# Kernel tuning notes

Hardware: AMD Instinct MI355X
Metric: run time of the kernel (lower is better)

Reference implementation:

```python
import jax, jax.numpy as jnp
import numpy as np

N_NODES = 40000


def _sage_conv(x, edge_index, W_l, W_r, b, num_nodes):
    # PyG SAGEConv (mean aggr): out = lin_l(mean_{j in N(i)} x_j) + lin_r(x_i)
    src, dst = edge_index[0], edge_index[1]
    msgs = x[src]                                            # [E, F] gather
    sums = jax.ops.segment_sum(msgs, dst, num_segments=num_nodes)
    counts = jax.ops.segment_sum(jnp.ones((src.shape[0],), x.dtype), dst,
                                 num_segments=num_nodes)
    mean = sums / jnp.maximum(counts, 1.0)[:, None]          # [N, F]
    return mean @ W_l + b + x @ W_r


def setup_inputs() -> dict:
    key = jax.random.key(0)
    ks = jax.random.split(key, 8)
    in_c, hid_c, out_c = 128, 256, 128
    x = jax.random.normal(ks[0], (N_NODES, in_c), dtype=jnp.float32)
    edge_index = jax.random.randint(ks[1], (2, 640000), 0, N_NODES, dtype=jnp.int64)
    s1 = 1.0 / np.sqrt(in_c)
    s2 = 1.0 / np.sqrt(hid_c)
    return {
        "x": x,
        "edge_index": edge_index,
        "W1_l": jax.random.uniform(ks[2], (in_c, hid_c), jnp.float32, -s1, s1),
        "W1_r": jax.random.uniform(ks[3], (in_c, hid_c), jnp.float32, -s1, s1),
        "b1": jnp.zeros((hid_c,), jnp.float32),
        "W2_l": jax.random.uniform(ks[4], (hid_c, out_c), jnp.float32, -s2, s2),
        "W2_r": jax.random.uniform(ks[5], (hid_c, out_c), jnp.float32, -s2, s2),
        "b2": jnp.zeros((out_c,), jnp.float32),
    }


def reference(x, edge_index, W1_l, W1_r, b1, W2_l, W2_r, b2):
    h = _sage_conv(x, edge_index, W1_l, W1_r, b1, N_NODES)
    h = jax.nn.relu(h)
    out = _sage_conv(h, edge_index, W2_l, W2_r, b2, N_NODES)
    return out
```

## Files before the change

### kernel.cpp

```cpp
#include <hip/hip_runtime.h>


constexpr int F1  = 128;
constexpr int HID = 256;

typedef __attribute__((ext_vector_type(8))) short   short8;
typedef __attribute__((ext_vector_type(8))) ushort  us8;
typedef __attribute__((ext_vector_type(4))) ushort  us4;
typedef __attribute__((ext_vector_type(4))) float   f32x4;

__device__ __forceinline__ ushort f2bf(float f) {
  unsigned u = __float_as_uint(f);
  return (ushort)((u + 0x7fffu + ((u >> 16) & 1u)) >> 16);
}
__device__ __forceinline__ float bf2f_lo(unsigned v) { return __uint_as_float(v << 16); }
__device__ __forceinline__ float bf2f_hi(unsigned v) { return __uint_as_float(v & 0xffff0000u); }

#define GLOAD_LDS16(gsrc, ldst)                                                  \
  __builtin_amdgcn_global_load_lds(                                              \
      (const __attribute__((address_space(1))) void*)(gsrc),                     \
      (__attribute__((address_space(3))) void*)(ldst), 16, 0, 0)

__global__ void prep_kernel(const float* __restrict__ x, ushort* __restrict__ Ab,
                            int* __restrict__ deg,
                            const float* __restrict__ W1l, const float* __restrict__ W1r,
                            const float* __restrict__ W2l, const float* __restrict__ W2r,
                            ushort* __restrict__ B1t, ushort* __restrict__ B2t, int N) {
  int i = blockIdx.x * blockDim.x + threadIdx.x;
  if (i < N) deg[i] = 0;
  if (i < N * 16) {
    int row = i >> 4, c = (i & 15) * 8;
    const float* p = x + (size_t)row * F1 + c;
    us8 o;
#pragma unroll
    for (int j = 0; j < 8; ++j) o[j] = f2bf(p[j]);
    *(us8*)(Ab + (size_t)row * HID + 128 + c) = o;
    return;
  }
  int j = i - N * 16;
  if (j >= 16384) return;
  int which = j >> 13;
  int jj = j & 8191;
  int n = jj >> 5;
  int kb = (jj & 31) * 8;
  us8 o;
  if (which == 0) {
#pragma unroll
    for (int q = 0; q < 8; ++q) {
      int k = kb + q;
      float v = (k < 128) ? W1l[k * HID + n] : W1r[(k - 128) * HID + n];
      o[q] = f2bf(v);
    }
    *(us8*)(B1t + n * HID + kb) = o;
  } else {
#pragma unroll
    for (int q = 0; q < 8; ++q) {
      int k = kb + q;
      float v = (n < 128) ? W2l[k * F1 + n] : W2r[k * F1 + (n - 128)];
      o[q] = f2bf(v);
    }
    *(us8*)(B2t + n * HID + kb) = o;
  }
}

__global__ void deg_kernel(const int* __restrict__ dst, int* __restrict__ deg, int E) {
  int i = (blockIdx.x * blockDim.x + threadIdx.x) * 4;
  if (i + 3 < E) {
    int4 d = *(const int4*)(dst + i);
    atomicAdd(deg + d.x, 1);
    atomicAdd(deg + d.y, 1);
    atomicAdd(deg + d.z, 1);
    atomicAdd(deg + d.w, 1);
  } else {
    for (int q = i; q < E && q < i + 4; ++q) atomicAdd(deg + dst[q], 1);
  }
}

__global__ __launch_bounds__(256) void scan_part(const int* __restrict__ deg,
                                                 int* __restrict__ bsum, int N) {
  __shared__ int sm[256];
  int t = threadIdx.x;
  int base = blockIdx.x * 1024 + t * 4;
  int s = 0;
  if (base + 3 < N) {
    int4 v = *(const int4*)(deg + base);
    s = v.x + v.y + v.z + v.w;
  } else {
    for (int q = 0; q < 4; ++q) if (base + q < N) s += deg[base + q];
  }
  sm[t] = s;
  __syncthreads();
  for (int d = 128; d; d >>= 1) {
    if (t < d) sm[t] += sm[t + d];
    __syncthreads();
  }
  if (t == 0) bsum[blockIdx.x] = sm[0];
}

__global__ __launch_bounds__(256) void scan_emit(const int* __restrict__ deg,
                                                 const int* __restrict__ bsum,
                                                 int* __restrict__ off,
                                                 int* __restrict__ cursor, int N, int nb) {
  __shared__ int sm[256];
  __shared__ int sboff;
  int t = threadIdx.x;
  if (t < 64) {
    int v = (t < nb) ? bsum[t] : 0;
    int inc = v;
    for (int d = 1; d < 64; d <<= 1) {
      int u = __shfl_up(inc, d);
      if (t >= d) inc += u;
    }
    if (t == (int)blockIdx.x) sboff = inc - v;
    if ((int)blockIdx.x == (int)gridDim.x - 1 && t == 63) off[N] = inc;
  }
  int base = blockIdx.x * 1024 + t * 4;
  int d0 = 0, d1 = 0, d2 = 0, d3 = 0;
  if (base + 3 < N) {
    int4 v = *(const int4*)(deg + base);
    d0 = v.x; d1 = v.y; d2 = v.z; d3 = v.w;
  } else {
    if (base + 0 < N) d0 = deg[base + 0];
    if (base + 1 < N) d1 = deg[base + 1];
    if (base + 2 < N) d2 = deg[base + 2];
    if (base + 3 < N) d3 = deg[base + 3];
  }
  int s = d0 + d1 + d2 + d3;
  sm[t] = s;
  __syncthreads();
  for (int d = 1; d < 256; d <<= 1) {
    int u = (t >= d) ? sm[t - d] : 0;
    __syncthreads();
    sm[t] += u;
    __syncthreads();
  }
  int o0 = (t ? sm[t - 1] : 0) + sboff;
  int o1 = o0 + d0, o2 = o1 + d1, o3 = o2 + d2;
  if (base + 3 < N) {
    int4 o = make_int4(o0, o1, o2, o3);
    *(int4*)(off + base) = o;
    *(int4*)(cursor + base) = o;
  } else {
    if (base + 0 < N) { off[base + 0] = o0; cursor[base + 0] = o0; }
    if (base + 1 < N) { off[base + 1] = o1; cursor[base + 1] = o1; }
    if (base + 2 < N) { off[base + 2] = o2; cursor[base + 2] = o2; }
    if (base + 3 < N) { off[base + 3] = o3; cursor[base + 3] = o3; }
  }
}

__global__ void fill_kernel(const int* __restrict__ src, const int* __restrict__ dst,
                            int* __restrict__ cursor, int* __restrict__ csr, int E) {
  int i = (blockIdx.x * blockDim.x + threadIdx.x) * 2;
  if (i + 1 < E) {
    int2 d = *(const int2*)(dst + i);
    int2 s = *(const int2*)(src + i);
    int p0 = atomicAdd(cursor + d.x, 1);
    csr[p0] = s.x;
    int p1 = atomicAdd(cursor + d.y, 1);
    csr[p1] = s.y;
  } else if (i < E) {
    int p = atomicAdd(cursor + dst[i], 1);
    csr[p] = src[i];
  }
}

__device__ __forceinline__ void acc8(float* acc, const uint4 v) {
  acc[0] += bf2f_lo(v.x); acc[1] += bf2f_hi(v.x);
  acc[2] += bf2f_lo(v.y); acc[3] += bf2f_hi(v.y);
  acc[4] += bf2f_lo(v.z); acc[5] += bf2f_hi(v.z);
  acc[6] += bf2f_lo(v.w); acc[7] += bf2f_hi(v.w);
}

__global__ __launch_bounds__(256) void agg1_kernel(const int* __restrict__ off,
                                                   const int* __restrict__ csr,
                                                   ushort* __restrict__ Ab, int N) {
  const int t = threadIdx.x;
  const int w = t >> 6, l = t & 63;
  const int g = l >> 4, sub = l & 15;
  const int node = blockIdx.x * 16 + w * 4 + g;
  if (node >= N) return;
  const int s = off[node], e = off[node + 1];
  float acc[8] = {0.f, 0.f, 0.f, 0.f, 0.f, 0.f, 0.f, 0.f};
  const int cb = sub * 8;
  const int4* csr4 = (const int4*)csr;
  int k0 = s & ~7;
  int4 c0 = csr4[(k0 >> 2) + 0];
  int4 c1 = csr4[(k0 >> 2) + 1];
#define ROW1(j) (*(const uint4*)(Ab + (size_t)(j) * HID + 128 + cb))
  for (int k = k0; k < e; k += 8) {
    int4 n0 = csr4[(k >> 2) + 2];
    int4 n1 = csr4[(k >> 2) + 3];
    if (k + 0 >= s && k + 0 < e) acc8(acc, ROW1(c0.x));
    if (k + 1 >= s && k + 1 < e) acc8(acc, ROW1(c0.y));
    if (k + 2 >= s && k + 2 < e) acc8(acc, ROW1(c0.z));
    if (k + 3 >= s && k + 3 < e) acc8(acc, ROW1(c0.w));
    if (k + 4 >= s && k + 4 < e) acc8(acc, ROW1(c1.x));
    if (k + 5 >= s && k + 5 < e) acc8(acc, ROW1(c1.y));
    if (k + 6 >= s && k + 6 < e) acc8(acc, ROW1(c1.z));
    if (k + 7 < e)               acc8(acc, ROW1(c1.w));
    c0 = n0; c1 = n1;
  }
#undef ROW1
  int d = e - s; if (d < 1) d = 1;
  float inv = 1.0f / (float)d;
  us8 o;
#pragma unroll
  for (int q = 0; q < 8; ++q) o[q] = f2bf(acc[q] * inv);
  *(us8*)(Ab + (size_t)node * HID + cb) = o;
}

__global__ __launch_bounds__(256) void agg2_kernel(const ushort* __restrict__ y2,
                                                   const int* __restrict__ off,
                                                   const int* __restrict__ csr,
                                                   float* __restrict__ out, int N) {
  const int t = threadIdx.x;
  const int w = t >> 6, l = t & 63;
  const int g = l >> 4, sub = l & 15;
  const int node = blockIdx.x * 16 + w * 4 + g;
  if (node >= N) return;
  const int s = off[node], e = off[node + 1];
  float acc[8] = {0.f, 0.f, 0.f, 0.f, 0.f, 0.f, 0.f, 0.f};
  const int cb = sub * 8;
  const int4* csr4 = (const int4*)csr;
  int k0 = s & ~7;
  int4 c0 = csr4[(k0 >> 2) + 0];
  int4 c1 = csr4[(k0 >> 2) + 1];
#define ROW2(j) (*(const uint4*)(y2 + (size_t)(j) * F1 + cb))
  for (int k = k0; k < e; k += 8) {
    int4 n0 = csr4[(k >> 2) + 2];
    int4 n1 = csr4[(k >> 2) + 3];
    if (k + 0 >= s && k + 0 < e) acc8(acc, ROW2(c0.x));
    if (k + 1 >= s && k + 1 < e) acc8(acc, ROW2(c0.y));
    if (k + 2 >= s && k + 2 < e) acc8(acc, ROW2(c0.z));
    if (k + 3 >= s && k + 3 < e) acc8(acc, ROW2(c0.w));
    if (k + 4 >= s && k + 4 < e) acc8(acc, ROW2(c1.x));
    if (k + 5 >= s && k + 5 < e) acc8(acc, ROW2(c1.y));
    if (k + 6 >= s && k + 6 < e) acc8(acc, ROW2(c1.z));
    if (k + 7 < e)               acc8(acc, ROW2(c1.w));
    c0 = n0; c1 = n1;
  }
#undef ROW2
  int d = e - s; if (d < 1) d = 1;
  float inv = 1.0f / (float)d;
  float* po = out + (size_t)node * F1 + cb;
  float4 z0 = *(const float4*)(po);
  float4 z1 = *(const float4*)(po + 4);
  z0.x += acc[0] * inv; z0.y += acc[1] * inv; z0.z += acc[2] * inv; z0.w += acc[3] * inv;
  z1.x += acc[4] * inv; z1.y += acc[5] * inv; z1.z += acc[6] * inv; z1.w += acc[7] * inv;
  *(float4*)(po)     = z0;
  *(float4*)(po + 4) = z1;
}

__global__ __launch_bounds__(256) void mlp_kernel(
    const ushort* __restrict__ A, const ushort* __restrict__ B1t,
    const ushort* __restrict__ B2t, const float* __restrict__ b1,
    const float* __restrict__ b2, ushort* __restrict__ y2,
    float* __restrict__ outp, int M) {
  constexpr int K = 256, BK = 64;
  __shared__ __align__(16) ushort hs[64 * 256];
  __shared__ __align__(16) ushort xreg[4096 + 16384];
  ushort* As  = xreg;
  ushort* B1s = xreg + 4096;
  ushort* B2s = xreg;
  const int t = threadIdx.x;
  const int l = t & 63;
  const int w = t >> 6;
  const int m0 = blockIdx.x * 64;
  const int wc = w * 64;
  const int sk = (((l & 7) ^ (l >> 3)) << 3);
  const int rsub = l >> 3;

  f32x4 acc[4][4];
  const f32x4 zero = {0.f, 0.f, 0.f, 0.f};
#pragma unroll
  for (int mi = 0; mi < 4; ++mi)
#pragma unroll
    for (int ni = 0; ni < 4; ++ni) acc[mi][ni] = zero;

  for (int k0 = 0; k0 < K; k0 += BK) {
    if (k0) __syncthreads();
#pragma unroll
    for (int q = 0; q < 2; ++q) {
      int r = w * 16 + q * 8 + rsub;
      int ar = m0 + r; if (ar >= M) ar = M - 1;
      GLOAD_LDS16(A + (size_t)ar * K + k0 + sk, &As[w * 1024 + q * 512]);
    }
#pragma unroll
    for (int q = 0; q < 8; ++q) {
      int r = w * 64 + q * 8 + rsub;
      GLOAD_LDS16(B1t + (size_t)r * K + k0 + sk, &B1s[w * 4096 + q * 512]);
    }
    __syncthreads();
#pragma unroll
    for (int ks = 0; ks < 2; ++ks) {
      short8 af[4], bfr[4];
      const int kin = ks * 64 + ((l >> 4) << 4);
#pragma unroll
      for (int i = 0; i < 4; ++i) {
        int rA = i * 16 + (l & 15);
        af[i] = *(const short8*)((const char*)As + rA * 128 + (kin ^ ((rA & 7) << 4)));
        int rB = wc + i * 16 + (l & 15);
        bfr[i] = *(const short8*)((const char*)B1s + rB * 128 + (kin ^ ((rB & 7) << 4)));
      }
#pragma unroll
      for (int mi = 0; mi < 4; ++mi)
#pragma unroll
        for (int ni = 0; ni < 4; ++ni)
          acc[mi][ni] = __builtin_amdgcn_mfma_f32_16x16x32_bf16(bfr[ni], af[mi], acc[mi][ni], 0, 0, 0);
    }
  }
#pragma unroll
  for (int ni = 0; ni < 4; ++ni) {
    const int cn = wc + ni * 16 + ((l >> 4) << 2);
    float4 bb = *(const float4*)(b1 + cn);
#pragma unroll
    for (int mi = 0; mi < 4; ++mi) {
      int row = mi * 16 + (l & 15);
      f32x4 v = acc[mi][ni];
      unsigned p0 = (unsigned)f2bf(fmaxf(v[0] + bb.x, 0.f)) |
                    ((unsigned)f2bf(fmaxf(v[1] + bb.y, 0.f)) << 16);
      unsigned p1 = (unsigned)f2bf(fmaxf(v[2] + bb.z, 0.f)) |
                    ((unsigned)f2bf(fmaxf(v[3] + bb.w, 0.f)) << 16);
      int byte = row * 512 + ((2 * cn) ^ ((row & 7) << 4));
      uint2 pk; pk.x = p0; pk.y = p1;
      *(uint2*)((char*)hs + byte) = pk;
      acc[mi][ni] = zero;
    }
  }
  __syncthreads();

  for (int k0 = 0; k0 < K; k0 += BK) {
    if (k0) __syncthreads();
#pragma unroll
    for (int q = 0; q < 8; ++q) {
      int r = w * 64 + q * 8 + rsub;
      GLOAD_LDS16(B2t + (size_t)r * K + k0 + sk, &B2s[w * 4096 + q * 512]);
    }
    __syncthreads();
#pragma unroll
    for (int ks = 0; ks < 2; ++ks) {
      short8 af[4], bfr[4];
      const int kin = ks * 64 + ((l >> 4) << 4);
#pragma unroll
      for (int i = 0; i < 4; ++i) {
        int rA = i * 16 + (l & 15);
        af[i] = *(const short8*)((const char*)hs + rA * 512 + ((2 * k0 + kin) ^ ((rA & 7) << 4)));
        int rB = wc + i * 16 + (l & 15);
        bfr[i] = *(const short8*)((const char*)B2s + rB * 128 + (kin ^ ((rB & 7) << 4)));
      }
#pragma unroll
      for (int mi = 0; mi < 4; ++mi)
#pragma unroll
        for (int ni = 0; ni < 4; ++ni)
          acc[mi][ni] = __builtin_amdgcn_mfma_f32_16x16x32_bf16(bfr[ni], af[mi], acc[mi][ni], 0, 0, 0);
    }
  }
#pragma unroll
  for (int ni = 0; ni < 4; ++ni) {
    const int cn = wc + ni * 16 + ((l >> 4) << 2);
    if (wc < 128) {
#pragma unroll
      for (int mi = 0; mi < 4; ++mi) {
        int row = m0 + mi * 16 + (l & 15);
        if (row >= M) continue;
        f32x4 v = acc[mi][ni];
        us4 o;
        o[0] = f2bf(v[0]); o[1] = f2bf(v[1]); o[2] = f2bf(v[2]); o[3] = f2bf(v[3]);
        *(us4*)(y2 + (size_t)row * F1 + cn) = o;
      }
    } else {
      float4 bb = *(const float4*)(b2 + (cn - 128));
#pragma unroll
      for (int mi = 0; mi < 4; ++mi) {
        int row = m0 + mi * 16 + (l & 15);
        if (row >= M) continue;
        f32x4 v = acc[mi][ni];
        float4 o;
        o.x = v[0] + bb.x; o.y = v[1] + bb.y; o.z = v[2] + bb.z; o.w = v[3] + bb.w;
        *(float4*)(outp + (size_t)row * F1 + (cn - 128)) = o;
      }
    }
  }
}

extern "C" void kernel_launch(void* const* d_in, const int* in_sizes, int n_in,
                              void* d_out, int out_size, void* d_ws, size_t ws_size,
                              hipStream_t stream) {
  const float* x   = (const float*)d_in[0];
  const int* edge  = (const int*)d_in[1];
  const float* W1l = (const float*)d_in[2];
  const float* W1r = (const float*)d_in[3];
  const float* b1  = (const float*)d_in[4];
  const float* W2l = (const float*)d_in[5];
  const float* W2r = (const float*)d_in[6];
  const float* b2  = (const float*)d_in[7];
  float* out = (float*)d_out;

  const int N = in_sizes[0] / F1;
  const int E = in_sizes[1] / 2;
  const int* src = edge;
  const int* dst = edge + E;

  uintptr_t p = (uintptr_t)d_ws;
  auto alloc = [&](size_t bytes) -> void* {
    void* r = (void*)p;
    p += (bytes + 255) & ~(size_t)255;
    return r;
  };
  int* deg      = (int*)alloc((size_t)N * 4);
  int* off      = (int*)alloc((size_t)(N + 1) * 4);
  int* cursor   = (int*)alloc((size_t)N * 4);
  int* csr      = (int*)alloc((size_t)(E + 16) * 4);
  int* bsum     = (int*)alloc(64 * 4);
  ushort* Abf   = (ushort*)alloc((size_t)N * HID * 2);
  ushort* y2    = (ushort*)alloc((size_t)N * F1 * 2);
  ushort* B1t   = (ushort*)alloc((size_t)HID * HID * 2);
  ushort* B2t   = (ushort*)alloc((size_t)HID * HID * 2);
  (void)ws_size; (void)n_in; (void)out_size;

  prep_kernel<<<(N * 16 + 16384 + 255) / 256, 256, 0, stream>>>(
      x, Abf, deg, W1l, W1r, W2l, W2r, B1t, B2t, N);
  deg_kernel<<<(E / 4 + 255) / 256, 256, 0, stream>>>(dst, deg, E);

  const int nb = (N + 1023) / 1024;
  scan_part<<<nb, 256, 0, stream>>>(deg, bsum, N);
  scan_emit<<<nb, 256, 0, stream>>>(deg, bsum, off, cursor, N, nb);

  fill_kernel<<<(E / 2 + 255) / 256, 256, 0, stream>>>(src, dst, cursor, csr, E);
  agg1_kernel<<<(N + 15) / 16, 256, 0, stream>>>(off, csr, Abf, N);

  mlp_kernel<<<(N + 63) / 64, 256, 0, stream>>>(Abf, B1t, B2t, b1, b2, y2, out, N);

  agg2_kernel<<<(N + 15) / 16, 256, 0, stream>>>(y2, off, csr, out, N);
}
```

Measured before the change: 235.6 us.

## Load GEMM operands directly from global memory into registers, dropping LDS staging

```diff
diff --git a/kernel.cpp b/kernel.cpp
--- a/kernel.cpp
+++ b/kernel.cpp
@@ -15,11 +15,6 @@
 }
 __device__ __forceinline__ float bf2f_lo(unsigned v) { return __uint_as_float(v << 16); }
 __device__ __forceinline__ float bf2f_hi(unsigned v) { return __uint_as_float(v & 0xffff0000u); }
-
-#define GLOAD_LDS16(gsrc, ldst)                                                  \
-  __builtin_amdgcn_global_load_lds(                                              \
-      (const __attribute__((address_space(1))) void*)(gsrc),                     \
-      (__attribute__((address_space(3))) void*)(ldst), 16, 0, 0)
 
 __global__ void prep_kernel(const float* __restrict__ x, ushort* __restrict__ Ab,
                             int* __restrict__ deg,
@@ -256,19 +251,14 @@
     const ushort* __restrict__ B2t, const float* __restrict__ b1,
     const float* __restrict__ b2, ushort* __restrict__ y2,
     float* __restrict__ outp, int M) {
-  constexpr int K = 256, BK = 64;
   __shared__ __align__(16) ushort hs[64 * 256];
-  __shared__ __align__(16) ushort xreg[4096 + 16384];
-  ushort* As  = xreg;
-  ushort* B1s = xreg + 4096;
-  ushort* B2s = xreg;
   const int t = threadIdx.x;
   const int l = t & 63;
   const int w = t >> 6;
   const int m0 = blockIdx.x * 64;
   const int wc = w * 64;
-  const int sk = (((l & 7) ^ (l >> 3)) << 3);
-  const int rsub = l >> 3;
+  const int lm = l & 15;
+  const int kg = l >> 4;
 
   f32x4 acc[4][4];
   const f32x4 zero = {0.f, 0.f, 0.f, 0.f};
@@ -277,45 +267,29 @@
 #pragma unroll
     for (int ni = 0; ni < 4; ++ni) acc[mi][ni] = zero;
 
-  for (int k0 = 0; k0 < K; k0 += BK) {
-    if (k0) __syncthreads();
-#pragma unroll
-    for (int q = 0; q < 2; ++q) {
-      int r = w * 16 + q * 8 + rsub;
-      int ar = m0 + r; if (ar >= M) ar = M - 1;
-      GLOAD_LDS16(A + (size_t)ar * K + k0 + sk, &As[w * 1024 + q * 512]);
-    }
-#pragma unroll
-    for (int q = 0; q < 8; ++q) {
-      int r = w * 64 + q * 8 + rsub;
-      GLOAD_LDS16(B1t + (size_t)r * K + k0 + sk, &B1s[w * 4096 + q * 512]);
-    }
-    __syncthreads();
-#pragma unroll
-    for (int ks = 0; ks < 2; ++ks) {
-      short8 af[4], bfr[4];
-      const int kin = ks * 64 + ((l >> 4) << 4);
-#pragma unroll
-      for (int i = 0; i < 4; ++i) {
-        int rA = i * 16 + (l & 15);
-        af[i] = *(const short8*)((const char*)As + rA * 128 + (kin ^ ((rA & 7) << 4)));
-        int rB = wc + i * 16 + (l & 15);
-        bfr[i] = *(const short8*)((const char*)B1s + rB * 128 + (kin ^ ((rB & 7) << 4)));
-      }
-#pragma unroll
-      for (int mi = 0; mi < 4; ++mi)
-#pragma unroll
-        for (int ni = 0; ni < 4; ++ni)
-          acc[mi][ni] = __builtin_amdgcn_mfma_f32_16x16x32_bf16(bfr[ni], af[mi], acc[mi][ni], 0, 0, 0);
-    }
-  }
+  for (int ks = 0; ks < 8; ++ks) {
+    const int kof = ks * 32 + kg * 8;
+    short8 af[4], bfr[4];
+#pragma unroll
+    for (int i = 0; i < 4; ++i) {
+      int row = m0 + i * 16 + lm; if (row >= M) row = M - 1;
+      af[i]  = *(const short8*)(A + (size_t)row * HID + kof);
+      bfr[i] = *(const short8*)(B1t + (size_t)(wc + i * 16 + lm) * HID + kof);
+    }
+#pragma unroll
+    for (int mi = 0; mi < 4; ++mi)
+#pragma unroll
+      for (int ni = 0; ni < 4; ++ni)
+        acc[mi][ni] = __builtin_amdgcn_mfma_f32_16x16x32_bf16(bfr[ni], af[mi], acc[mi][ni], 0, 0, 0);
+  }
+
 #pragma unroll
   for (int ni = 0; ni < 4; ++ni) {
-    const int cn = wc + ni * 16 + ((l >> 4) << 2);
+    const int cn = wc + ni * 16 + (kg << 2);
     float4 bb = *(const float4*)(b1 + cn);
 #pragma unroll
     for (int mi = 0; mi < 4; ++mi) {
-      int row = mi * 16 + (l & 15);
+      int row = mi * 16 + lm;
       f32x4 v = acc[mi][ni];
       unsigned p0 = (unsigned)f2bf(fmaxf(v[0] + bb.x, 0.f)) |
                     ((unsigned)f2bf(fmaxf(v[1] + bb.y, 0.f)) << 16);
@@ -329,39 +303,29 @@
   }
   __syncthreads();
 
-  for (int k0 = 0; k0 < K; k0 += BK) {
-    if (k0) __syncthreads();
-#pragma unroll
-    for (int q = 0; q < 8; ++q) {
-      int r = w * 64 + q * 8 + rsub;
-      GLOAD_LDS16(B2t + (size_t)r * K + k0 + sk, &B2s[w * 4096 + q * 512]);
-    }
-    __syncthreads();
-#pragma unroll
-    for (int ks = 0; ks < 2; ++ks) {
-      short8 af[4], bfr[4];
-      const int kin = ks * 64 + ((l >> 4) << 4);
-#pragma unroll
-      for (int i = 0; i < 4; ++i) {
-        int rA = i * 16 + (l & 15);
-        af[i] = *(const short8*)((const char*)hs + rA * 512 + ((2 * k0 + kin) ^ ((rA & 7) << 4)));
-        int rB = wc + i * 16 + (l & 15);
-        bfr[i] = *(const short8*)((const char*)B2s + rB * 128 + (kin ^ ((rB & 7) << 4)));
-      }
-#pragma unroll
-      for (int mi = 0; mi < 4; ++mi)
-#pragma unroll
-        for (int ni = 0; ni < 4; ++ni)
-          acc[mi][ni] = __builtin_amdgcn_mfma_f32_16x16x32_bf16(bfr[ni], af[mi], acc[mi][ni], 0, 0, 0);
-    }
-  }
+  for (int ks = 0; ks < 8; ++ks) {
+    const int kof = ks * 32 + kg * 8;
+    short8 af[4], bfr[4];
+#pragma unroll
+    for (int i = 0; i < 4; ++i) {
+      int rA = i * 16 + lm;
+      af[i]  = *(const short8*)((const char*)hs + rA * 512 + ((2 * kof) ^ ((rA & 7) << 4)));
+      bfr[i] = *(const short8*)(B2t + (size_t)(wc + i * 16 + lm) * HID + kof);
+    }
+#pragma unroll
+    for (int mi = 0; mi < 4; ++mi)
+#pragma unroll
+      for (int ni = 0; ni < 4; ++ni)
+        acc[mi][ni] = __builtin_amdgcn_mfma_f32_16x16x32_bf16(bfr[ni], af[mi], acc[mi][ni], 0, 0, 0);
+  }
+
 #pragma unroll
   for (int ni = 0; ni < 4; ++ni) {
-    const int cn = wc + ni * 16 + ((l >> 4) << 2);
+    const int cn = wc + ni * 16 + (kg << 2);
     if (wc < 128) {
 #pragma unroll
       for (int mi = 0; mi < 4; ++mi) {
-        int row = m0 + mi * 16 + (l & 15);
+        int row = m0 + mi * 16 + lm;
         if (row >= M) continue;
         f32x4 v = acc[mi][ni];
         us4 o;
@@ -372,7 +336,7 @@
       float4 bb = *(const float4*)(b2 + (cn - 128));
 #pragma unroll
       for (int mi = 0; mi < 4; ++mi) {
-        int row = m0 + mi * 16 + (l & 15);
+        int row = m0 + mi * 16 + lm;
         if (row >= M) continue;
         f32x4 v = acc[mi][ni];
         float4 o;
```

Result: slower. 251.6 us (+6.8%).
